# Optimization experiments

Hardware: AMD Instinct MI355X
Metric: run time of the kernel (lower is better)

## Reference

```python
import jax, jax.numpy as jnp
import numpy as np

N, E, G = 50000, 600000, 256
IN_C, EMB, HID, OUT = 64, 128, 128, 36


def _glorot(key, fan_in, fan_out):
    lim = np.sqrt(6.0 / (fan_in + fan_out)).astype(np.float32)
    return jax.random.uniform(key, (fan_in, fan_out), jnp.float32, -lim, lim)


def setup_inputs() -> dict:
    key = jax.random.key(0)
    ks = jax.random.split(key, 12)
    x = jax.random.normal(ks[0], (N, IN_C), jnp.float32)
    edge_index = jax.random.randint(ks[1], (2, E), 0, N, jnp.int64)
    edge_attr = jax.random.uniform(ks[2], (E,), jnp.float32)
    # deterministic sorted batch assignment -> every graph id 0..G-1 is nonempty
    batch = ((jnp.arange(N, dtype=jnp.int64) * G) // N).astype(jnp.int64)
    rho = jax.random.uniform(ks[3], (G,), jnp.float32)
    return {
        "x": x,
        "edge_attr": edge_attr,
        "rho": rho,
        "conv0_w": _glorot(ks[4], IN_C, EMB),
        "conv0_b": jnp.zeros((EMB,), jnp.float32),
        "conv1_w": _glorot(ks[5], EMB, EMB),
        "conv1_b": jnp.zeros((EMB,), jnp.float32),
        "mlp0_w": _glorot(ks[6], 2 * EMB + 1, HID),
        "mlp0_b": jnp.zeros((HID,), jnp.float32),
        "mlp1_w": _glorot(ks[7], HID, HID),
        "mlp1_b": jnp.zeros((HID,), jnp.float32),
        "out_w": _glorot(ks[8], HID, OUT),
        "out_b": jnp.zeros((OUT,), jnp.float32),
        "edge_index": edge_index,
        "batch": batch,
    }


def _gcn_conv(h, row, col, w, W, b):
    # PyG GCNConv: self-loops already appended in (row, col, w).
    deg = jax.ops.segment_sum(w, col, num_segments=N)  # in-degree by edge weight
    dis = jnp.where(deg > 0, jax.lax.rsqrt(jnp.maximum(deg, 1e-30)), 0.0)
    norm = dis[row] * w * dis[col]                     # [E+N]
    h = h @ W                                          # [N, out]
    msg = norm[:, None] * h[row]                       # gather + scale
    return jax.ops.segment_sum(msg, col, num_segments=N) + b


def reference(x, edge_attr, rho, conv0_w, conv0_b, conv1_w, conv1_b,
              mlp0_w, mlp0_b, mlp1_w, mlp1_b, out_w, out_b,
              edge_index, batch):
    # add self-loops with weight 1
    loops = jnp.arange(N, dtype=edge_index.dtype)
    row = jnp.concatenate([edge_index[0], loops])
    col = jnp.concatenate([edge_index[1], loops])
    w = jnp.concatenate([edge_attr, jnp.ones((N,), edge_attr.dtype)])

    h = jax.nn.relu(_gcn_conv(x, row, col, w, conv0_w, conv0_b))
    h = jax.nn.relu(_gcn_conv(h, row, col, w, conv1_w, conv1_b))

    gmp = jax.ops.segment_max(h, batch, num_segments=G)             # [G, EMB]
    cnt = jax.ops.segment_sum(jnp.ones((N,), h.dtype), batch, num_segments=G)
    gap = jax.ops.segment_sum(h, batch, num_segments=G) / cnt[:, None]
    hg = jnp.concatenate([gmp, gap, rho[:, None]], axis=1)          # [G, 2*EMB+1]

    hg = jax.nn.relu(hg @ mlp0_w + mlp0_b)
    hg = jax.nn.relu(hg @ mlp1_w + mlp1_b)
    return hg @ out_w + out_b
```

## Files before the change

### kernel.cpp

```cpp
#include <hip/hip_runtime.h>
#include <hip/hip_fp16.h>
#include <math.h>

using half8 = __attribute__((ext_vector_type(8))) _Float16;
using f32x4 = __attribute__((ext_vector_type(4))) float;

#define CAP 64


__device__ __forceinline__ float wdec(unsigned int v) {
    __half h;
    *reinterpret_cast<unsigned short*>(&h) = (unsigned short)(v >> 16);
    return __half2float(h);
}

__device__ __forceinline__ unsigned int wenc(int src, float w) {
    __half h = __float2half(w);
    return (unsigned int)src |
           ((unsigned int)(*reinterpret_cast<unsigned short*>(&h)) << 16);
}

__device__ __forceinline__ void st_half4(__half* p, float4 v) {
    __half2 a = __floats2half2_rn(v.x, v.y);
    __half2 b = __floats2half2_rn(v.z, v.w);
    int2 raw;
    raw.x = *reinterpret_cast<int*>(&a);
    raw.y = *reinterpret_cast<int*>(&b);
    *reinterpret_cast<int2*>(p) = raw;
}


__global__ void k_setup(const float* __restrict__ w0, __half* __restrict__ wt0,
                        const float* __restrict__ w1, __half* __restrict__ wt1,
                        int* __restrict__ cursor, int n) {
    int i = blockIdx.x * blockDim.x + threadIdx.x;
    if (i < 64 * 128) {
        int k = i >> 7, c = i & 127;
        wt0[c * 64 + k] = __float2half(w0[i]);
    }
    if (i < 128 * 128) {
        int k = i >> 7, c = i & 127;
        wt1[c * 128 + k] = __float2half(w1[i]);
    }
    if (i < n) cursor[i] = 0;
}


__global__ void k_place(const int* __restrict__ row, const int* __restrict__ col,
                        const float* __restrict__ w, int* __restrict__ cursor,
                        unsigned int* __restrict__ slab, int e) {
    int base = (blockIdx.x * blockDim.x + threadIdx.x) * 4;
    if (base + 3 < e) {
        int4 r4 = *reinterpret_cast<const int4*>(&row[base]);
        int4 c4 = *reinterpret_cast<const int4*>(&col[base]);
        float4 w4 = *reinterpret_cast<const float4*>(&w[base]);
        int s0 = atomicAdd(&cursor[c4.x], 1);
        int s1 = atomicAdd(&cursor[c4.y], 1);
        int s2 = atomicAdd(&cursor[c4.z], 1);
        int s3 = atomicAdd(&cursor[c4.w], 1);
        if (s0 < CAP) slab[(size_t)c4.x * CAP + s0] = wenc(r4.x, w4.x);
        if (s1 < CAP) slab[(size_t)c4.y * CAP + s1] = wenc(r4.y, w4.y);
        if (s2 < CAP) slab[(size_t)c4.z * CAP + s2] = wenc(r4.z, w4.z);
        if (s3 < CAP) slab[(size_t)c4.w * CAP + s3] = wenc(r4.w, w4.w);
    } else {
        for (int i = base; i < e; ++i) {
            int c = col[i];
            int s = atomicAdd(&cursor[c], 1);
            if (s < CAP) slab[(size_t)c * CAP + s] = wenc(row[i], w[i]);
        }
    }
}

__global__ __launch_bounds__(256) void k_degscale(
    const unsigned int* __restrict__ slab, const int* __restrict__ cursor,
    const float* __restrict__ x, float* __restrict__ dis,
    __half* __restrict__ xs, int n)
{
    __shared__ float sdis[256];
    int t = threadIdx.x;
    int base = blockIdx.x * 256;
    int i = base + t;
    if (i < n) {
        int cnt = min(cursor[i], CAP);
        float s = 1.0f;
        const unsigned int* p = &slab[(size_t)i * CAP];
        for (int j = 0; j < cnt; ++j) s += wdec(p[j]);
        float d = rsqrtf(s);
        dis[i] = d;
        sdis[t] = d;
    }
    __syncthreads();
#pragma unroll
    for (int it = 0; it < 16; ++it) {
        int id = it * 256 + t;
        int node_l = id >> 4;
        if (base + node_l < n) {
            float d = sdis[node_l];
            float4 v = reinterpret_cast<const float4*>(x)[(size_t)base * 16 + id];
            v.x *= d; v.y *= d; v.z *= d; v.w *= d;
            st_half4(&xs[((size_t)base * 16 + id) * 4], v);
        }
    }
}


template<int K, bool SC>
__global__ __launch_bounds__(256) void k_agg_gemm(
    const __half* __restrict__ hs, const unsigned int* __restrict__ slab,
    const int* __restrict__ cursor, const float* __restrict__ dis,
    const __half* __restrict__ wt, const float* __restrict__ bias,
    __half* __restrict__ out, int n)
{
    constexpr int SA = K + 8;
    constexpr int CPR = K / 8;
    constexpr int CW = K / 4;
    __shared__ _Float16 Al[64 * SA];
    __shared__ _Float16 Wl[128 * SA];
    const int tid = threadIdx.x;
    const int row0 = blockIdx.x * 64;

#pragma unroll
    for (int it = 0; it < (128 * CPR) / 256; ++it) {
        int id = tid + it * 256;
        int c = id / CPR, kc = id % CPR;
        int4 raw = *reinterpret_cast<const int4*>(&wt[(size_t)c * K + kc * 8]);
        *reinterpret_cast<int4*>(&Wl[c * SA + kc * 8]) = raw;
    }

    {
        const int lr = tid >> 2, part = tid & 3;
        const int node = row0 + lr;
        const int c0 = part * CW;
        if (node < n) {
            float acc[CW];
#pragma unroll
            for (int cc = 0; cc < CW / 8; ++cc) {
                half8 v = *reinterpret_cast<const half8*>(&hs[(size_t)node * K + c0 + cc * 8]);
#pragma unroll
                for (int u = 0; u < 8; ++u) acc[cc * 8 + u] = (float)v[u];
            }
            int cnt = min(cursor[node], CAP);
            const unsigned int* sp = &slab[(size_t)node * CAP];
            for (int j = 0; j < cnt; ++j) {
                unsigned int rec = sp[j];
                int src = rec & 0xFFFF;
                float w = wdec(rec);
#pragma unroll
                for (int cc = 0; cc < CW / 8; ++cc) {
                    half8 v = *reinterpret_cast<const half8*>(&hs[(size_t)src * K + c0 + cc * 8]);
#pragma unroll
                    for (int u = 0; u < 8; ++u)
                        acc[cc * 8 + u] = fmaf(w, (float)v[u], acc[cc * 8 + u]);
                }
            }
            float d = dis[node];
#pragma unroll
            for (int cc = 0; cc < CW / 8; ++cc) {
                half8 hv;
#pragma unroll
                for (int u = 0; u < 8; ++u) hv[u] = (_Float16)(d * acc[cc * 8 + u]);
                *reinterpret_cast<half8*>(&Al[lr * SA + c0 + cc * 8]) = hv;
            }
        }
    }
    __syncthreads();

    const int l = tid & 63, w = tid >> 6;
    const int r = l & 15, kg = l >> 4;

    f32x4 acc[8];
#pragma unroll
    for (int ct = 0; ct < 8; ++ct) acc[ct] = (f32x4){0.f, 0.f, 0.f, 0.f};

#pragma unroll
    for (int kst = 0; kst < K / 32; ++kst) {
        half8 af = *reinterpret_cast<const half8*>(&Al[(16 * w + r) * SA + kst * 32 + kg * 8]);
#pragma unroll
        for (int ct = 0; ct < 8; ++ct) {
            half8 bf = *reinterpret_cast<const half8*>(&Wl[(16 * ct + r) * SA + kst * 32 + kg * 8]);
            acc[ct] = __builtin_amdgcn_mfma_f32_16x16x32_f16(af, bf, acc[ct], 0, 0, 0);
        }
    }

    float sc[4];
#pragma unroll
    for (int q = 0; q < 4; ++q) {
        int gr = row0 + 16 * w + kg * 4 + q;
        sc[q] = (SC && gr < n) ? dis[gr] : 1.0f;
    }
#pragma unroll
    for (int ct = 0; ct < 8; ++ct) {
        float bv = bias[16 * ct + r];
#pragma unroll
        for (int q = 0; q < 4; ++q) {
            int gr = row0 + 16 * w + kg * 4 + q;
            if (gr < n) {
                float v = fmaxf(acc[ct][q] + bv, 0.f);
                if constexpr (SC) v *= sc[q];
                out[(size_t)gr * 128 + 16 * ct + r] = __float2half(v);
            }
        }
    }
}


__device__ __forceinline__ int lowbound(const int* __restrict__ b, int n, int key) {
    int lo = 0, hi = n;
    while (lo < hi) { int mid = (lo + hi) >> 1; if (b[mid] < key) lo = mid + 1; else hi = mid; }
    return lo;
}

#define NSLICE 8

__global__ __launch_bounds__(128) void k_pool_part(
    const __half* __restrict__ h, const int* __restrict__ batch,
    float* __restrict__ part, int n)
{
    int g = blockIdx.x >> 3, s = blockIdx.x & (NSLICE - 1);
    int ch = threadIdx.x;
    __shared__ int sbeg, send;
    if (ch == 0) {
        sbeg = lowbound(batch, n, g);
        send = lowbound(batch, n, g + 1);
    }
    __syncthreads();
    float mx = -INFINITY, sm = 0.f;
    for (int i = sbeg + s; i < send; i += NSLICE) {
        float v = __half2float(h[(size_t)i * 128 + ch]);
        mx = fmaxf(mx, v);
        sm += v;
    }
    size_t base = ((size_t)g * NSLICE + s) * 256;
    part[base + ch] = mx;
    part[base + 128 + ch] = sm;
}


__global__ __launch_bounds__(256) void k_head_mlp(
    const float* __restrict__ part, const int* __restrict__ batch,
    const float* __restrict__ rho,
    const float* __restrict__ w0, const float* __restrict__ b0,
    const float* __restrict__ w1, const float* __restrict__ b1,
    const float* __restrict__ w2, const float* __restrict__ b2,
    float* __restrict__ out, int n)
{
    int g = blockIdx.x;
    int tid = threadIdx.x;
    int ch = tid & 127, half = tid >> 7;
    __shared__ float hg[257];
    __shared__ float t0[128];
    __shared__ float red[2][128];
    __shared__ int scnt;
    if (tid == 0) {
        int beg = lowbound(batch, n, g);
        int end = lowbound(batch, n, g + 1);
        scnt = end - beg;
        hg[256] = rho[g];
    }
    {
        float mx = -INFINITY, sm = 0.f;
        for (int s = half * (NSLICE / 2); s < (half + 1) * (NSLICE / 2); ++s) {
            size_t base = ((size_t)g * NSLICE + s) * 256;
            mx = fmaxf(mx, part[base + ch]);
            sm += part[base + 128 + ch];
        }
        red[half][ch] = mx;
        __syncthreads();
        if (half == 0) {
            float m2 = fmaxf(mx, red[1][ch]);
            hg[ch] = m2;
            red[0][ch] = sm;
        }
        __syncthreads();
        if (half == 1) red[1][ch] = sm + red[0][ch];
        __syncthreads();
        if (half == 0) hg[128 + ch] = red[1][ch] / (float)scnt;
        __syncthreads();
    }
    {
        float a = 0.f, b = 0.f;
        int j0 = half * 128;
        int jend = half ? 257 : 128;
        int j = j0;
        for (; j + 2 <= jend; j += 2) {
            a = fmaf(hg[j], w0[(size_t)j * 128 + ch], a);
            b = fmaf(hg[j + 1], w0[(size_t)(j + 1) * 128 + ch], b);
        }
        if (j < jend) a = fmaf(hg[j], w0[(size_t)j * 128 + ch], a);
        red[half][ch] = a + b;
        __syncthreads();
        if (half == 0) t0[ch] = fmaxf(red[0][ch] + red[1][ch] + b0[ch], 0.f);
        __syncthreads();
    }
    {
        float a = 0.f, b = 0.f;
        int j0 = half * 64;
        for (int j = j0; j < j0 + 64; j += 2) {
            a = fmaf(t0[j], w1[(size_t)j * 128 + ch], a);
            b = fmaf(t0[j + 1], w1[(size_t)(j + 1) * 128 + ch], b);
        }
        red[half][ch] = a + b;
        __syncthreads();
        if (half == 0) hg[ch] = fmaxf(red[0][ch] + red[1][ch] + b1[ch], 0.f);
        __syncthreads();
    }
    if (ch < 36) {
        float a = 0.f, b = 0.f;
        int j0 = half * 64;
        for (int j = j0; j < j0 + 64; j += 2) {
            a = fmaf(hg[j], w2[(size_t)j * 36 + ch], a);
            b = fmaf(hg[j + 1], w2[(size_t)(j + 1) * 36 + ch], b);
        }
        red[half][ch] = a + b;
    }
    __syncthreads();
    if (half == 0 && ch < 36)
        out[(size_t)g * 36 + ch] = red[0][ch] + red[1][ch] + b2[ch];
}


extern "C" void kernel_launch(void* const* d_in, const int* in_sizes, int n_in,
                              void* d_out, int out_size, void* d_ws, size_t ws_size,
                              hipStream_t stream)
{
    const float* x        = (const float*)d_in[0];
    const float* edge_attr= (const float*)d_in[1];
    const float* rho      = (const float*)d_in[2];
    const float* conv0_w  = (const float*)d_in[3];
    const float* conv0_b  = (const float*)d_in[4];
    const float* conv1_w  = (const float*)d_in[5];
    const float* conv1_b  = (const float*)d_in[6];
    const float* mlp0_w   = (const float*)d_in[7];
    const float* mlp0_b   = (const float*)d_in[8];
    const float* mlp1_w   = (const float*)d_in[9];
    const float* mlp1_b   = (const float*)d_in[10];
    const float* out_w    = (const float*)d_in[11];
    const float* out_b    = (const float*)d_in[12];
    const int*   edge_idx = (const int*)d_in[13];
    const int*   batch    = (const int*)d_in[14];

    const int N = in_sizes[0] / 64;
    const int E = in_sizes[1];
    const int G = in_sizes[2];
    const int* erow = edge_idx;
    const int* ecol = edge_idx + E;

    char* ws = (char*)d_ws;
    size_t off = 0;
    auto alloc = [&](size_t bytes) -> void* {
        off = (off + 255) & ~(size_t)255;
        void* p = ws + off;
        off += bytes;
        return p;
    };
    float*        dis    = (float*)alloc((size_t)N * 4);
    int*          cursor = (int*)  alloc((size_t)N * 4);
    unsigned int* slab   = (unsigned int*)alloc((size_t)N * CAP * 4);
    __half*       bufA   = (__half*)alloc((size_t)N * 128 * 2);
    __half*       bufB   = (__half*)alloc((size_t)N * 128 * 2);
    float*        part   = (float*)alloc((size_t)G * NSLICE * 256 * 4);
    __half*       wt0    = (__half*)alloc((size_t)64 * 128 * 2);
    __half*       wt1    = (__half*)alloc((size_t)128 * 128 * 2);

    dim3 b256(256);
    int setup_n = (N > 128 * 128) ? N : 128 * 128;
    k_setup<<<(setup_n + 255) / 256, b256, 0, stream>>>(conv0_w, wt0, conv1_w, wt1, cursor, N);
    k_place<<<((E + 3) / 4 + 255) / 256, b256, 0, stream>>>(erow, ecol, edge_attr, cursor, slab, E);
    k_degscale<<<(N + 255) / 256, b256, 0, stream>>>(slab, cursor, x, dis, bufA, N);

    k_agg_gemm<64, true><<<(N + 63) / 64, b256, 0, stream>>>(bufA, slab, cursor, dis, wt0, conv0_b, bufB, N);
    k_agg_gemm<128, false><<<(N + 63) / 64, b256, 0, stream>>>(bufB, slab, cursor, dis, wt1, conv1_b, bufA, N);

    k_pool_part<<<G * NSLICE, dim3(128), 0, stream>>>(bufA, batch, part, N);
    k_head_mlp<<<G, b256, 0, stream>>>(part, batch, rho,
                                       mlp0_w, mlp0_b, mlp1_w, mlp1_b, out_w, out_b,
                                       (float*)d_out, N);
}
```

Baseline: 166.6 us.

## Simplify edge placement, vectorize degree sum, read GEMM weights directly from global

```diff
diff --git a/kernel.cpp b/kernel.cpp
--- a/kernel.cpp
+++ b/kernel.cpp
@@ -49,25 +49,11 @@
 __global__ void k_place(const int* __restrict__ row, const int* __restrict__ col,
                         const float* __restrict__ w, int* __restrict__ cursor,
                         unsigned int* __restrict__ slab, int e) {
-    int base = (blockIdx.x * blockDim.x + threadIdx.x) * 4;
-    if (base + 3 < e) {
-        int4 r4 = *reinterpret_cast<const int4*>(&row[base]);
-        int4 c4 = *reinterpret_cast<const int4*>(&col[base]);
-        float4 w4 = *reinterpret_cast<const float4*>(&w[base]);
-        int s0 = atomicAdd(&cursor[c4.x], 1);
-        int s1 = atomicAdd(&cursor[c4.y], 1);
-        int s2 = atomicAdd(&cursor[c4.z], 1);
-        int s3 = atomicAdd(&cursor[c4.w], 1);
-        if (s0 < CAP) slab[(size_t)c4.x * CAP + s0] = wenc(r4.x, w4.x);
-        if (s1 < CAP) slab[(size_t)c4.y * CAP + s1] = wenc(r4.y, w4.y);
-        if (s2 < CAP) slab[(size_t)c4.z * CAP + s2] = wenc(r4.z, w4.z);
-        if (s3 < CAP) slab[(size_t)c4.w * CAP + s3] = wenc(r4.w, w4.w);
-    } else {
-        for (int i = base; i < e; ++i) {
-            int c = col[i];
-            int s = atomicAdd(&cursor[c], 1);
-            if (s < CAP) slab[(size_t)c * CAP + s] = wenc(row[i], w[i]);
-        }
+    int i = blockIdx.x * blockDim.x + threadIdx.x;
+    if (i < e) {
+        int c = col[i];
+        int s = atomicAdd(&cursor[c], 1);
+        if (s < CAP) slab[(size_t)c * CAP + s] = wenc(row[i], w[i]);
     }
 }
 
@@ -84,7 +70,12 @@
         int cnt = min(cursor[i], CAP);
         float s = 1.0f;
         const unsigned int* p = &slab[(size_t)i * CAP];
-        for (int j = 0; j < cnt; ++j) s += wdec(p[j]);
+        int j = 0;
+        for (; j + 4 <= cnt; j += 4) {
+            uint4 rec = *reinterpret_cast<const uint4*>(&p[j]);
+            s += wdec(rec.x) + wdec(rec.y) + wdec(rec.z) + wdec(rec.w);
+        }
+        for (; j < cnt; ++j) s += wdec(p[j]);
         float d = rsqrtf(s);
         dis[i] = d;
         sdis[t] = d;
@@ -112,20 +103,10 @@
     __half* __restrict__ out, int n)
 {
     constexpr int SA = K + 8;
-    constexpr int CPR = K / 8;
     constexpr int CW = K / 4;
     __shared__ _Float16 Al[64 * SA];
-    __shared__ _Float16 Wl[128 * SA];
     const int tid = threadIdx.x;
     const int row0 = blockIdx.x * 64;
-
-#pragma unroll
-    for (int it = 0; it < (128 * CPR) / 256; ++it) {
-        int id = tid + it * 256;
-        int c = id / CPR, kc = id % CPR;
-        int4 raw = *reinterpret_cast<const int4*>(&wt[(size_t)c * K + kc * 8]);
-        *reinterpret_cast<int4*>(&Wl[c * SA + kc * 8]) = raw;
-    }
 
     {
         const int lr = tid >> 2, part = tid & 3;
@@ -177,7 +158,7 @@
         half8 af = *reinterpret_cast<const half8*>(&Al[(16 * w + r) * SA + kst * 32 + kg * 8]);
 #pragma unroll
         for (int ct = 0; ct < 8; ++ct) {
-            half8 bf = *reinterpret_cast<const half8*>(&Wl[(16 * ct + r) * SA + kst * 32 + kg * 8]);
+            half8 bf = *reinterpret_cast<const half8*>(&wt[(size_t)(16 * ct + r) * K + kst * 32 + kg * 8]);
             acc[ct] = __builtin_amdgcn_mfma_f32_16x16x32_f16(af, bf, acc[ct], 0, 0, 0);
         }
     }
@@ -365,7 +346,7 @@
     dim3 b256(256);
     int setup_n = (N > 128 * 128) ? N : 128 * 128;
     k_setup<<<(setup_n + 255) / 256, b256, 0, stream>>>(conv0_w, wt0, conv1_w, wt1, cursor, N);
-    k_place<<<((E + 3) / 4 + 255) / 256, b256, 0, stream>>>(erow, ecol, edge_attr, cursor, slab, E);
+    k_place<<<(E + 255) / 256, b256, 0, stream>>>(erow, ecol, edge_attr, cursor, slab, E);
     k_degscale<<<(N + 255) / 256, b256, 0, stream>>>(slab, cursor, x, dis, bufA, N);
 
     k_agg_gemm<64, true><<<(N + 63) / 64, b256, 0, stream>>>(bufA, slab, cursor, dis, wt0, conv0_b, bufB, N);
```

After: 165.2 us. About the same (-0.9%).
